# Optimization experiments

Measured on AMD Instinct MI355X. Metric: run time of the kernel, lower is better.

Reference implementation:

```python
import jax, jax.numpy as jnp
import numpy as np
from jax import lax

NEG = -1e30  # safe -inf surrogate (avoids nan grads)
CTC_WEIGHT = 0.3


def _excl_cumsum(e):
    # exclusive cumsum along last axis: (..., U) -> (..., U+1)
    c = jnp.cumsum(e, axis=-1)
    return jnp.concatenate([jnp.zeros_like(c[..., :1]), c], axis=-1)


def _rnnt_loss(log_probs, targets, frame_len, tgt_len, blank):
    """RNNT forward DP. log_probs: (B,T,U+1,V) log-softmaxed. Returns per-seq NLL (B,)."""
    B, T, U1, V = log_probs.shape
    blank_lp = log_probs[..., blank]  # (B,T,U1)
    emit = jnp.take_along_axis(log_probs[:, :, :U1 - 1, :],
                               targets[:, None, :, None], axis=3)[..., 0]  # (B,T,U)
    # alpha[0,u] = sum_{j<u} emit[0,j]
    alpha0 = _excl_cumsum(emit[:, 0])  # (B,U1)

    def step(alpha_prev, inp):
        blank_prev, emit_t = inp  # (B,U1), (B,U)
        a = alpha_prev + blank_prev
        # alpha[t,u] = LSE(a_u, alpha[t,u-1] + emit[t,u-1]) solved in closed form:
        # alpha[t,u] = E[u] + cumLSE_{k<=u}(a_k - E[k]),  E = exclusive cumsum of emit
        E = _excl_cumsum(emit_t)
        alpha_t = E + lax.associative_scan(jnp.logaddexp, a - E, axis=-1)
        return alpha_t, alpha_t

    xs = (jnp.swapaxes(blank_lp[:, :-1], 0, 1), jnp.swapaxes(emit[:, 1:], 0, 1))
    _, alphas = lax.scan(step, alpha0, xs)
    alphas = jnp.concatenate([alpha0[None], alphas], axis=0)  # (T,B,U1)
    bi = jnp.arange(B)
    t_idx = frame_len - 1
    ll = alphas[t_idx, bi, tgt_len] + blank_lp[bi, t_idx, tgt_len]
    return -ll


def _ctc_loss(log_probs, targets, frame_len, tgt_len, blank):
    """CTC forward DP. log_probs: (B,T,V) log-softmaxed. Returns per-seq NLL (B,)."""
    B, T, V = log_probs.shape
    U = targets.shape[1]
    S = 2 * U + 1
    ext = jnp.full((B, S), blank, dtype=targets.dtype).at[:, 1::2].set(targets)  # (B,S)
    lp_ext = jnp.take_along_axis(log_probs, ext[:, None, :], axis=2)  # (B,T,S)
    ext_m2 = jnp.pad(ext[:, :-2], ((0, 0), (2, 0)), constant_values=blank)
    can_skip = (jnp.arange(S)[None, :] >= 2) & (ext != blank) & (ext != ext_m2)
    alpha0 = jnp.full((B, S), NEG).at[:, 0].set(lp_ext[:, 0, 0]).at[:, 1].set(lp_ext[:, 0, 1])

    def step(alpha, lp_t):
        p1 = jnp.pad(alpha[:, :-1], ((0, 0), (1, 0)), constant_values=NEG)
        p2 = jnp.where(can_skip,
                       jnp.pad(alpha[:, :-2], ((0, 0), (2, 0)), constant_values=NEG), NEG)
        m = jnp.maximum(jnp.maximum(alpha, p1), p2)
        new = lp_t + m + jnp.log(jnp.exp(alpha - m) + jnp.exp(p1 - m) + jnp.exp(p2 - m))
        return new, new

    _, alphas = lax.scan(step, alpha0, jnp.swapaxes(lp_ext, 0, 1)[1:])
    alphas = jnp.concatenate([alpha0[None], alphas], axis=0)  # (T,B,S)
    bi = jnp.arange(B)
    t_idx = frame_len - 1
    a_last = alphas[t_idx, bi, 2 * tgt_len]
    a_prev = alphas[t_idx, bi, 2 * tgt_len - 1]
    return -jnp.logaddexp(a_last, a_prev)


def setup_inputs() -> dict:
    key = jax.random.key(0)
    ks = jax.random.split(key, 9)
    B, T, U, V = 4, 200, 50, 1024
    D, H = 512, 640
    return {
        "x_enc": jax.random.normal(ks[0], (B, T, D), jnp.float32),
        "x_dec": jax.random.normal(ks[1], (B, U + 1, H), jnp.float32),
        "target": jax.random.randint(ks[2], (B, U), 0, V - 1),  # excludes blank = V-1
        "frame_length": jax.random.randint(ks[3], (B,), 150, T + 1).astype(jnp.int32),
        "target_length": jax.random.randint(ks[4], (B,), 30, U + 1).astype(jnp.int32),
        "W_ctc": jax.random.normal(ks[5], (D, V), jnp.float32) * 0.02,
        "b_ctc": jnp.zeros((V,), jnp.float32),
        "W_enc": jax.random.normal(ks[6], (D, H), jnp.float32) * 0.02,
        "W_pred": jax.random.normal(ks[7], (H, H), jnp.float32) * 0.02,
        "b_joint": jnp.zeros((H,), jnp.float32),
        "W_out": jax.random.normal(ks[8], (H, V), jnp.float32) * 0.02,
        "b_out": jnp.zeros((V,), jnp.float32),
    }


def reference(x_enc, x_dec, target, frame_length, target_length,
              W_ctc, b_ctc, W_enc, W_pred, b_joint, W_out, b_out):
    B = x_enc.shape[0]
    V = W_ctc.shape[1]
    blank = V - 1
    # CTC head: linear + log_softmax over vocab
    ctc_lp = jax.nn.log_softmax(x_enc @ W_ctc + b_ctc, axis=-1)  # (B,T,V)
    # Joiner: enc proj (B,T,1,J) + pred proj (B,1,U+1,J) -> tanh -> vocab
    joint = jnp.tanh(jnp.einsum('btd,dj->btj', x_enc, W_enc)[:, :, None, :]
                     + jnp.einsum('buh,hj->buj', x_dec, W_pred)[:, None, :, :]
                     + b_joint)  # (B,T,U+1,J)
    rnnt_lp = jax.nn.log_softmax(jnp.einsum('btuj,jv->btuv', joint, W_out) + b_out, axis=-1)
    rnnt = _rnnt_loss(rnnt_lp, target, frame_length, target_length, blank).mean()
    ctc = _ctc_loss(ctc_lp, target, frame_length, target_length, blank).sum() / B
    return rnnt + CTC_WEIGHT * ctc
```

## Files before the change

kernel.cpp:

```cpp
#include <hip/hip_runtime.h>
#include <hip/hip_bf16.h>

typedef __bf16 bf16_t;
typedef __attribute__((ext_vector_type(8))) __bf16 bf16x8;
typedef __attribute__((ext_vector_type(4))) float f32x4;
typedef __attribute__((ext_vector_type(8))) int i32x8;
typedef __attribute__((ext_vector_type(4))) int i32x4;

#define NEGV (-1e30f)

#define BB 4
#define TT 200
#define UU 50
#define U1 51
#define VV 1024
#define DD 512
#define HH 640
#define RTOT (BB*TT*U1)
#define NBLK 638
#define SS 101

__device__ __forceinline__ float lae(float a, float b) {
    float mx = fmaxf(a, b);
    return mx + __logf(__expf(a - mx) + __expf(b - mx));
}
__device__ __forceinline__ float lae3(float a, float b, float c) {
    float mx = fmaxf(fmaxf(a, b), c);
    return mx + __logf(__expf(a - mx) + __expf(b - mx) + __expf(c - mx));
}
__device__ __forceinline__ float tanh_rcp(float x) {
    x = fminf(fmaxf(x, -10.f), 10.f);
    float ex = __expf(2.f * x);
    float r = __builtin_amdgcn_rcpf(ex + 1.f);
    return (ex - 1.f) * r;
}

__device__ __forceinline__ void pack_seg(const float* __restrict__ W, bf16_t* __restrict__ Wf,
                                         int e, int K32, int N)
{
    int j  = e & 7;
    int l  = (e >> 3) & 63;
    int kk = (e >> 9) % K32;
    int nt = e / (K32 * 512);
    int v = nt * 16 + (l & 15);
    int k = kk * 32 + ((l >> 4) << 2) + (j & 3) + ((j >> 2) << 4);
    Wf[e] = (bf16_t)W[(size_t)k * N + v];
}

__device__ __forceinline__ void pack_out8_mx(const float* __restrict__ W, unsigned* __restrict__ Wf8,
                                             int e32)
{
    int w4   = e32 & 7;
    int l    = (e32 >> 3) & 63;
    int ksnt = e32 >> 9;
    int ks   = ksnt % 5;
    int nt   = ksnt / 5;
    int v = nt * 16 + (l & 15);
    int kb = ks * 128 + ((l >> 4) << 5) + w4 * 4;
    float f[4];
#pragma unroll
    for (int t = 0; t < 4; ++t) f[t] = W[(size_t)(kb + t) * VV + v] * 16.f;
    unsigned r = __builtin_amdgcn_cvt_pk_fp8_f32(f[0], f[1], 0, false);
    r = __builtin_amdgcn_cvt_pk_fp8_f32(f[2], f[3], r, true);
    Wf8[e32] = r;
}

__global__ void pack_bf16(const float* __restrict__ Wenc, const float* __restrict__ Wpred,
                          const float* __restrict__ Wctc,
                          bf16_t* __restrict__ FEnc, bf16_t* __restrict__ FPred,
                          bf16_t* __restrict__ FCtc, float* __restrict__ out)
{
    if (blockIdx.x == 0 && threadIdx.x == 0) out[0] = 0.f;
    int e = blockIdx.x * 256 + threadIdx.x;
    if (e < 327680) { pack_seg(Wenc, FEnc, e, 16, 640); return; }
    e -= 327680;
    if (e < 409600) { pack_seg(Wpred, FPred, e, 20, 640); return; }
    e -= 409600;
    pack_seg(Wctc, FCtc, e, 16, 1024);
}

template<int K32, int L, bool LSE, int J>
__device__ void gemm_dev(const float* __restrict__ A, int M, int rowbase, int K,
                         const bf16_t* __restrict__ Wf, const float* __restrict__ bias,
                         float* __restrict__ C, float* __restrict__ lse_out, int N,
                         bf16_t* Atile, float (*ps)[8])
{
    const int tid = threadIdx.x;
#pragma unroll
    for (int it = 0; it < J * K32 / 8; ++it) {
        int fi = it * 512 + tid;
        int l = fi & 63, jk = fi >> 6;
        int j = jk / K32, kk = jk - j * K32;
        int row = rowbase + j * 16 + (l & 15);
        if (row > M - 1) row = M - 1;
        int c0 = kk * 32 + ((l >> 4) << 2);
        const float4 a0 = *(const float4*)&A[(size_t)row * K + c0];
        const float4 a1 = *(const float4*)&A[(size_t)row * K + c0 + 16];
        bf16x8 v;
        v[0] = (bf16_t)a0.x; v[1] = (bf16_t)a0.y; v[2] = (bf16_t)a0.z; v[3] = (bf16_t)a0.w;
        v[4] = (bf16_t)a1.x; v[5] = (bf16_t)a1.y; v[6] = (bf16_t)a1.z; v[7] = (bf16_t)a1.w;
        *(bf16x8*)&Atile[(size_t)fi * 8] = v;
    }
    __syncthreads();

    const int l = tid & 63, w = tid >> 6;
    const int lrow = l & 15, lhi = l >> 4;

    f32x4 acc[J][L];
#pragma unroll
    for (int j = 0; j < J; ++j)
#pragma unroll
        for (int li = 0; li < L; ++li) acc[j][li] = f32x4{0.f, 0.f, 0.f, 0.f};

    for (int kk = 0; kk < K32; ++kk) {
        bf16x8 a[J];
#pragma unroll
        for (int j = 0; j < J; ++j)
            a[j] = *(const bf16x8*)&Atile[(size_t)(((j * K32 + kk) * 64 + l) * 8)];
#pragma unroll
        for (int li = 0; li < L; ++li) {
            bf16x8 b = *(const bf16x8*)&Wf[(size_t)(((w * L + li) * K32 + kk) * 64 + l) * 8];
#pragma unroll
            for (int j = 0; j < J; ++j)
                acc[j][li] = __builtin_amdgcn_mfma_f32_16x16x32_bf16(a[j], b, acc[j][li], 0, 0, 0);
        }
    }

    float se[J][4];
    if (LSE) {
#pragma unroll
        for (int j = 0; j < J; ++j)
#pragma unroll
            for (int i = 0; i < 4; ++i) se[j][i] = 0.f;
    }
#pragma unroll
    for (int j = 0; j < J; ++j)
#pragma unroll
        for (int li = 0; li < L; ++li) {
            int col = (w * L + li) * 16 + lrow;
            float bv = bias ? bias[col] : 0.f;
#pragma unroll
            for (int i = 0; i < 4; ++i) {
                int grow = rowbase + 16 * j + lhi * 4 + i;
                float x = acc[j][li][i] + bv;
                if (grow < M) C[(size_t)grow * N + col] = x;
                if (LSE) se[j][i] += __expf(x);
            }
        }
    if (LSE) {
#pragma unroll
        for (int d = 1; d < 16; d <<= 1)
#pragma unroll
            for (int j = 0; j < J; ++j)
#pragma unroll
                for (int i = 0; i < 4; ++i) se[j][i] += __shfl_xor(se[j][i], d);
        if (lrow == 0) {
#pragma unroll
            for (int j = 0; j < J; ++j)
#pragma unroll
                for (int i = 0; i < 4; ++i) ps[16 * j + lhi * 4 + i][w] = se[j][i];
        }
        __syncthreads();
        if (tid < J * 16) {
            float s = 0.f;
#pragma unroll
            for (int w0 = 0; w0 < 8; ++w0) s += ps[tid][w0];
            int grow = rowbase + tid;
            if (grow < M) lse_out[grow] = __logf(s);
        }
    }
}

__global__ __launch_bounds__(512)
void mfma_gemm3(const float* __restrict__ x_enc, const float* __restrict__ x_dec,
                const bf16_t* __restrict__ FEnc, const bf16_t* __restrict__ FPred,
                const bf16_t* __restrict__ FCtc, const float* __restrict__ b_ctc,
                float* __restrict__ enc_proj, float* __restrict__ pred_proj,
                float* __restrict__ ctc_logits, float* __restrict__ ctc_lse,
                const float* __restrict__ Wout, unsigned* __restrict__ FOut8)
{
    __shared__ bf16_t Atile[2560 * 8];
    __shared__ float ps[64][8];
    int blk = blockIdx.x;
    if (blk >= 107) {
        int e = (blk - 107) * 512 + threadIdx.x;
        pack_out8_mx(Wout, FOut8, e);
        return;
    }
    if (blk < 50)
        gemm_dev<16, 5, false, 1>(x_enc, 800, blk * 16, 512, FEnc, nullptr, enc_proj, nullptr, 640, Atile, ps);
    else if (blk < 57)
        gemm_dev<20, 5, false, 2>(x_dec, 204, (blk - 50) * 32, 640, FPred, nullptr, pred_proj, nullptr, 640, Atile, ps);
    else
        gemm_dev<16, 8, true, 1>(x_enc, 800, (blk - 57) * 16, 512, FCtc, b_ctc, ctc_logits, ctc_lse, 1024, Atile, ps);
}

__global__ __launch_bounds__(512)
void joint_gemm(const float* __restrict__ enc,
                const float* __restrict__ pred,
                const float* __restrict__ bj,
                const unsigned* __restrict__ Wf8,
                const float* __restrict__ bo,
                const int* __restrict__ target,
                float* __restrict__ blank_buf, float* __restrict__ emit_buf)
{
    __shared__ __align__(16) char tile[64 * 656];
    __shared__ __align__(16) char Afrag8[40960];
    __shared__ const float* ep[64];
    __shared__ const float* pp[64];
    const int tid = threadIdx.x;
    const int blk = blockIdx.x;

    const int l = tid & 63, w = tid >> 6;
    const int lrow = l & 15, lhi = l >> 4;

    if (tid < 64) {
        int r = blk * 64 + tid; if (r > RTOT - 1) r = RTOT - 1;
        int b = r / (TT * U1); int rem = r - b * (TT * U1);
        int t = rem / U1;      int u = rem - t * U1;
        ep[tid] = enc + (size_t)(b * TT + t) * HH;
        pp[tid] = pred + (size_t)(b * U1 + u) * HH;
    }
    __syncthreads();

#pragma unroll 4
    for (int it = 0; it < 20; ++it) {
        int i = it * 512 + tid;
        int row = i / 160;
        int c4 = i - row * 160;
        int c0 = c4 * 4;
        const float4 e4 = *(const float4*)&ep[row][c0];
        const float4 p4 = *(const float4*)&pp[row][c0];
        const float4 q4 = *(const float4*)&bj[c0];
        float f0 = tanh_rcp(e4.x + p4.x + q4.x);
        float f1 = tanh_rcp(e4.y + p4.y + q4.y);
        float f2 = tanh_rcp(e4.z + p4.z + q4.z);
        float f3 = tanh_rcp(e4.w + p4.w + q4.w);
        unsigned r0 = __builtin_amdgcn_cvt_pk_fp8_f32(f0, f1, 0, false);
        unsigned v = __builtin_amdgcn_cvt_pk_fp8_f32(f2, f3, r0, true);
        *(unsigned*)&tile[row * 656 + c0] = v;
    }
    __syncthreads();

#pragma unroll
    for (int it = 0; it < 5; ++it) {
        int c = it * 512 + tid;
        int lA = c & 63;
        int plane = c >> 6;
        int h = plane & 1;
        int jks = plane >> 1;
        int ks = jks % 5;
        int j = jks / 5;
        int row = j * 16 + (lA & 15);
        int kbase = ks * 128 + ((lA >> 4) << 5) + h * 16;
        uint4 v = *(const uint4*)&tile[row * 656 + kbase];
        *(uint4*)&Afrag8[(size_t)c * 16] = v;
    }
    __syncthreads();

    f32x4 acc[4][8];
#pragma unroll
    for (int j = 0; j < 4; ++j)
#pragma unroll
        for (int li = 0; li < 8; ++li) acc[j][li] = f32x4{0.f, 0.f, 0.f, 0.f};

    const char* Bp8 = (const char*)Wf8 + (size_t)(w * 8) * 10240 + (size_t)l * 32;

    const int rot = blk % 5;
    auto kstep = [&](int ks) {
        i32x8 a[4];
#pragma unroll
        for (int j = 0; j < 4; ++j) {
            i32x4 lo = *(const i32x4*)(Afrag8 + (size_t)(((j * 5 + ks) * 2 + 0) * 1024 + l * 16));
            i32x4 hi = *(const i32x4*)(Afrag8 + (size_t)(((j * 5 + ks) * 2 + 1) * 1024 + l * 16));
            a[j][0] = lo[0]; a[j][1] = lo[1]; a[j][2] = lo[2]; a[j][3] = lo[3];
            a[j][4] = hi[0]; a[j][5] = hi[1]; a[j][6] = hi[2]; a[j][7] = hi[3];
        }
#pragma unroll
        for (int li = 0; li < 8; ++li) {
            i32x8 b = *(const i32x8*)(Bp8 + (size_t)li * 10240 + (size_t)ks * 2048);
#pragma unroll
            for (int j = 0; j < 4; ++j)
                acc[j][li] = __builtin_amdgcn_mfma_scale_f32_16x16x128_f8f6f4(
                    a[j], b, acc[j][li], 0, 0,
                    0, 0x7F7F7F7F, 0, 0x7F7F7F7F);
        }
    };
    for (int ks0 = rot; ks0 < 5; ++ks0) kstep(ks0);
    for (int ks0 = 0; ks0 < rot; ++ks0) kstep(ks0);

    int tg[4][4];
#pragma unroll
    for (int j = 0; j < 4; ++j)
#pragma unroll
        for (int i = 0; i < 4; ++i) {
            int r = blk * 64 + 16 * j + lhi * 4 + i; if (r > RTOT - 1) r = RTOT - 1;
            int b = r / (TT * U1); int rem = r - b * (TT * U1);
            int u = rem % U1;
            tg[j][i] = (u < UU) ? target[b * UU + u] : -1;
        }

    float se[4][4], ee[4][4], bbv[4][4];
#pragma unroll
    for (int j = 0; j < 4; ++j)
#pragma unroll
        for (int i = 0; i < 4; ++i) { se[j][i] = 0.f; ee[j][i] = NEGV; bbv[j][i] = NEGV; }

#pragma unroll
    for (int li = 0; li < 8; ++li) {
        int col = (w * 8 + li) * 16 + lrow;
        float bv = bo[col];
#pragma unroll
        for (int j = 0; j < 4; ++j)
#pragma unroll
            for (int i = 0; i < 4; ++i) {
                float x = acc[j][li][i] * 0.0625f + bv;
                se[j][i] += __expf(x);
                if (col == tg[j][i]) ee[j][i] = x;
            }
    }
    if (w == 7) {
        float bv = bo[1023];
#pragma unroll
        for (int j = 0; j < 4; ++j)
#pragma unroll
            for (int i = 0; i < 4; ++i) {
                float x = acc[j][7][i] * 0.0625f + bv;
                if (lrow == 15) bbv[j][i] = x;
            }
    }
#pragma unroll
    for (int d = 1; d < 16; d <<= 1)
#pragma unroll
        for (int j = 0; j < 4; ++j)
#pragma unroll
            for (int i = 0; i < 4; ++i) {
                se[j][i] += __shfl_xor(se[j][i], d);
                ee[j][i] = fmaxf(ee[j][i], __shfl_xor(ee[j][i], d));
                bbv[j][i] = fmaxf(bbv[j][i], __shfl_xor(bbv[j][i], d));
            }

    __syncthreads();
    float (*ps)[8] = (float (*)[8])(Afrag8);
    float (*pe)[8] = (float (*)[8])(Afrag8 + 2048);
    float (*pb)[8] = (float (*)[8])(Afrag8 + 4096);
    if (lrow == 0) {
#pragma unroll
        for (int j = 0; j < 4; ++j)
#pragma unroll
            for (int i = 0; i < 4; ++i) {
                int r = 16 * j + lhi * 4 + i;
                ps[r][w] = se[j][i]; pe[r][w] = ee[j][i]; pb[r][w] = bbv[j][i];
            }
    }
    __syncthreads();
    if (tid < 64) {
        float s = 0.f, e = NEGV, bq = NEGV;
#pragma unroll
        for (int w0 = 0; w0 < 8; ++w0) {
            s += ps[tid][w0];
            e = fmaxf(e, pe[tid][w0]);
            bq = fmaxf(bq, pb[tid][w0]);
        }
        float lse = __logf(s);
        int gid = blk * 64 + tid;
        if (gid < RTOT) {
            blank_buf[gid] = bq - lse;
            emit_buf[gid]  = e - lse;
        }
    }
}

__global__ __launch_bounds__(256)
void dp_fused(const float* __restrict__ blank_buf, const float* __restrict__ emit_buf,
              const float* __restrict__ ctc_logits, const float* __restrict__ ctc_lse,
              const int* __restrict__ target, const int* __restrict__ frame_len,
              const int* __restrict__ tgt_len,
              float* __restrict__ out)
{
    __shared__ __align__(16) float sm[28416];
    const int bid = blockIdx.x;
    const int tid = threadIdx.x;

    if (bid < 4) {
        const int b = bid;
        float2* pk = (float2*)sm;
        for (int i = tid; i < TT * U1; i += 256) {
            int t = i / U1, uu = i - t * U1;
            float bl = blank_buf[(b * TT + t) * U1 + uu];
            float em = emit_buf[(b * TT + t) * U1 + uu];
            pk[uu * 217 + t + 8] = make_float2(bl, em);
        }
        __syncthreads();
        if (tid >= 64) return;
        const int u = tid;
        const int fl = frame_len[b], tl = tgt_len[b];
        const int dh = fl - 1 + tl;
        const bool isTL = (u == tl);
        const bool act = (u < U1);
        float A = (u == 0) ? 0.f : NEGV;
        float Asave = (dh == 0 && isTL) ? A : NEGV;
        const float2* prow = pk + u * 217;

        for (int d0 = 1; d0 <= 249; d0 += 8) {
            int tb = d0 - 1 - u;
            int tc = tb; if (tc < -8) tc = -8; if (tc > 200) tc = 200;
            float2 buf[8];
#pragma unroll
            for (int s = 0; s < 8; ++s) buf[s] = prow[tc + 8 + s];
#pragma unroll
            for (int s = 0; s < 8; ++s) {
                int d = d0 + s;
                int t_new = d - u;
                float2 be = buf[s];
                float vshare = A + be.y;
                float left = __shfl_up(vshare, 1);
                if (u == 0) left = NEGV;
                float up = (t_new >= 1) ? (A + be.x) : NEGV;
                float Anew = lae(up, left);
                bool valid = act && (t_new >= 0) && (t_new < TT);
                A = valid ? Anew : A;
                Asave = (isTL && d == dh) ? A : Asave;
            }
        }
        if (isTL && act) {
            float bl = prow[(fl - 1) + 8].x;
            atomicAdd(out, -0.25f * (Asave + bl));
        }
    } else {
        const int b = bid - 4;
        float* lpE = sm;
        float* lpO = sm + 208;
        for (int i = tid; i < TT; i += 256) {
            int bt = b * TT + i;
            lpE[i] = ctc_logits[(size_t)bt * VV + (VV - 1)] - ctc_lse[bt];
        }
        for (int i = tid; i < TT * UU; i += 256) {
            int t = i / UU, uu = i - t * UU;
            int bt = b * TT + t;
            lpO[uu * 209 + t] = ctc_logits[(size_t)bt * VV + target[b * UU + uu]] - ctc_lse[bt];
        }
        __syncthreads();
        if (tid >= 64) return;
        const int u = tid;
        const int fl = frame_len[b], tl = tgt_len[b];
        const bool acte = (u <= 50);
        const bool acto = (u < 50);
        bool skip = (u >= 1 && u < UU) ? (target[b * UU + u] != target[b * UU + u - 1]) : false;
        const float* orow = lpO + u * 209;
        float old_e = (u == 0) ? lpE[0] : NEGV;
        float old_o = (u == 0) ? orow[0] : NEGV;
        float Esave = (fl == 1) ? old_e : NEGV;
        float Osave = (fl == 1) ? old_o : NEGV;

        for (int t0 = 1; t0 <= 193; t0 += 8) {
            float bo8[8], be8[8];
#pragma unroll
            for (int s = 0; s < 8; ++s) { bo8[s] = orow[t0 + s]; be8[s] = lpE[t0 + s]; }
#pragma unroll
            for (int s = 0; s < 8; ++s) {
                int t = t0 + s;
                float prev_o = __shfl_up(old_o, 1);
                if (u == 0) prev_o = NEGV;
                float ne = be8[s] + lae(old_e, prev_o);
                float no = bo8[s] + lae3(old_o, old_e, skip ? prev_o : NEGV);
                old_e = acte ? ne : NEGV;
                old_o = acto ? no : NEGV;
                bool hv = (t == fl - 1) && (t < TT);
                Esave = hv ? old_e : Esave;
                Osave = hv ? old_o : Osave;
            }
        }
        float a_last = __shfl(Esave, tl);
        float a_prev = __shfl(Osave, tl - 1);
        if (u == 0) atomicAdd(out, -0.075f * lae(a_last, a_prev));
    }
}

extern "C" void kernel_launch(void* const* d_in, const int* in_sizes, int n_in,
                              void* d_out, int out_size, void* d_ws, size_t ws_size,
                              hipStream_t stream)
{
    const float* x_enc   = (const float*)d_in[0];
    const float* x_dec   = (const float*)d_in[1];
    const int*   target  = (const int*)d_in[2];
    const int*   frame_l = (const int*)d_in[3];
    const int*   tgt_l   = (const int*)d_in[4];
    const float* W_ctc   = (const float*)d_in[5];
    const float* b_ctc   = (const float*)d_in[6];
    const float* W_enc   = (const float*)d_in[7];
    const float* W_pred  = (const float*)d_in[8];
    const float* b_joint = (const float*)d_in[9];
    const float* W_out   = (const float*)d_in[10];
    const float* b_out   = (const float*)d_in[11];
    float* out = (float*)d_out;

    float* wsf        = (float*)d_ws;
    float* enc_proj   = wsf;
    float* pred_proj  = wsf + 512000;
    float* ctc_logits = wsf + 642560;
    float* ctc_lse    = wsf + 1461760;
    float* blank_buf  = wsf + 1462592;
    float* emit_buf   = wsf + 1503424;
    unsigned* FOut8 = (unsigned*)(wsf + 1544272);
    bf16_t* FEnc  = (bf16_t*)(wsf + 1708112);
    bf16_t* FPred = (bf16_t*)(wsf + 1871952);
    bf16_t* FCtc  = (bf16_t*)(wsf + 2076752);

    pack_bf16<<<4928, 256, 0, stream>>>(W_enc, W_pred, W_ctc, FEnc, FPred, FCtc, out);
    mfma_gemm3<<<427, 512, 0, stream>>>(x_enc, x_dec, FEnc, FPred, FCtc, b_ctc,
                                        enc_proj, pred_proj, ctc_logits, ctc_lse,
                                        W_out, FOut8);
    joint_gemm<<<NBLK, 512, 0, stream>>>(enc_proj, pred_proj, b_joint, FOut8, b_out,
                                         target, blank_buf, emit_buf);
    dp_fused<<<8, 256, 0, stream>>>(blank_buf, emit_buf, ctc_logits, ctc_lse,
                                    target, frame_l, tgt_l, out);
}
```

Measured before the change: 150.2 us.

## Overlap CTC DP with joint GEMM and vectorize bf16 weight packing

Moves the CTC forward DP out of the final DP kernel and into four extra blocks appended to the joint GEMM launch. The CTC recursion, which only needs the CTC logits, can then run concurrently with the joiner instead of serially after it. The bf16 weight pack kernel now has each thread produce 8 packed elements written with one vector store, cutting the grid eightfold. Risks: the joint kernel grows its shared allocation to a single union buffer, and the extra long-running serial blocks could extend the joint kernel's tail.

```diff
diff --git a/kernel.cpp b/kernel.cpp
--- a/kernel.cpp
+++ b/kernel.cpp
@@ -35,18 +35,6 @@
     return (ex - 1.f) * r;
 }
 
-__device__ __forceinline__ void pack_seg(const float* __restrict__ W, bf16_t* __restrict__ Wf,
-                                         int e, int K32, int N)
-{
-    int j  = e & 7;
-    int l  = (e >> 3) & 63;
-    int kk = (e >> 9) % K32;
-    int nt = e / (K32 * 512);
-    int v = nt * 16 + (l & 15);
-    int k = kk * 32 + ((l >> 4) << 2) + (j & 3) + ((j >> 2) << 4);
-    Wf[e] = (bf16_t)W[(size_t)k * N + v];
-}
-
 __device__ __forceinline__ void pack_out8_mx(const float* __restrict__ W, unsigned* __restrict__ Wf8,
                                              int e32)
 {
@@ -71,12 +59,23 @@
                           bf16_t* __restrict__ FCtc, float* __restrict__ out)
 {
     if (blockIdx.x == 0 && threadIdx.x == 0) out[0] = 0.f;
-    int e = blockIdx.x * 256 + threadIdx.x;
-    if (e < 327680) { pack_seg(Wenc, FEnc, e, 16, 640); return; }
-    e -= 327680;
-    if (e < 409600) { pack_seg(Wpred, FPred, e, 20, 640); return; }
-    e -= 409600;
-    pack_seg(Wctc, FCtc, e, 16, 1024);
+    int f = blockIdx.x * 256 + threadIdx.x;
+    const float* W; bf16_t* Wf; int K32, N;
+    if (f < 40960)      { W = Wenc;  Wf = FEnc;  K32 = 16; N = 640; }
+    else if (f < 92160) { f -= 40960; W = Wpred; Wf = FPred; K32 = 20; N = 640; }
+    else                { f -= 92160; W = Wctc;  Wf = FCtc;  K32 = 16; N = 1024; }
+    int l  = f & 63;
+    int kk = (f >> 6) % K32;
+    int nt = f / (64 * K32);
+    int v  = nt * 16 + (l & 15);
+    int kb = kk * 32 + ((l >> 4) << 2);
+    bf16x8 o;
+#pragma unroll
+    for (int j = 0; j < 8; ++j) {
+        int k = kb + (j & 3) + ((j >> 2) << 4);
+        o[j] = (bf16_t)W[(size_t)k * N + v];
+    }
+    *(bf16x8*)&Wf[(size_t)f * 8] = o;
 }
 
 template<int K32, int L, bool LSE, int J>
@@ -202,15 +201,69 @@
                 const unsigned* __restrict__ Wf8,
                 const float* __restrict__ bo,
                 const int* __restrict__ target,
-                float* __restrict__ blank_buf, float* __restrict__ emit_buf)
-{
-    __shared__ __align__(16) char tile[64 * 656];
-    __shared__ __align__(16) char Afrag8[40960];
+                float* __restrict__ blank_buf, float* __restrict__ emit_buf,
+                const float* __restrict__ ctc_logits, const float* __restrict__ ctc_lse,
+                const int* __restrict__ frame_len, const int* __restrict__ tgt_len,
+                float* __restrict__ out)
+{
+    __shared__ __align__(16) char smem[84992];
     __shared__ const float* ep[64];
     __shared__ const float* pp[64];
     const int tid = threadIdx.x;
     const int blk = blockIdx.x;
 
+    if (blk >= NBLK) {
+        const int b = blk - NBLK;
+        float* lpE = (float*)smem;
+        float* lpO = (float*)smem + 208;
+        for (int i = tid; i < TT; i += 512) {
+            int bt = b * TT + i;
+            lpE[i] = ctc_logits[(size_t)bt * VV + (VV - 1)] - ctc_lse[bt];
+        }
+        for (int i = tid; i < TT * UU; i += 512) {
+            int t = i / UU, uu = i - t * UU;
+            int bt = b * TT + t;
+            lpO[uu * 209 + t] = ctc_logits[(size_t)bt * VV + target[b * UU + uu]] - ctc_lse[bt];
+        }
+        __syncthreads();
+        if (tid >= 64) return;
+        const int u = tid;
+        const int fl = frame_len[b], tl = tgt_len[b];
+        const bool acte = (u <= 50);
+        const bool acto = (u < 50);
+        bool skip = (u >= 1 && u < UU) ? (target[b * UU + u] != target[b * UU + u - 1]) : false;
+        const float* orow = lpO + u * 209;
+        float old_e = (u == 0) ? lpE[0] : NEGV;
+        float old_o = (u == 0) ? orow[0] : NEGV;
+        float Esave = (fl == 1) ? old_e : NEGV;
+        float Osave = (fl == 1) ? old_o : NEGV;
+
+        for (int t0 = 1; t0 <= 193; t0 += 8) {
+            float bo8[8], be8[8];
+#pragma unroll
+            for (int s = 0; s < 8; ++s) { bo8[s] = orow[t0 + s]; be8[s] = lpE[t0 + s]; }
+#pragma unroll
+            for (int s = 0; s < 8; ++s) {
+                int t = t0 + s;
+                float prev_o = __shfl_up(old_o, 1);
+                if (u == 0) prev_o = NEGV;
+                float ne = be8[s] + lae(old_e, prev_o);
+                float no = bo8[s] + lae3(old_o, old_e, skip ? prev_o : NEGV);
+                old_e = acte ? ne : NEGV;
+                old_o = acto ? no : NEGV;
+                bool hv = (t == fl - 1) && (t < TT);
+                Esave = hv ? old_e : Esave;
+                Osave = hv ? old_o : Osave;
+            }
+        }
+        float a_last = __shfl(Esave, tl);
+        float a_prev = __shfl(Osave, tl - 1);
+        if (u == 0) atomicAdd(out, -0.075f * lae(a_last, a_prev));
+        return;
+    }
+
+    char* tile = smem;
+    char* Afrag8 = smem + 41984;
     const int l = tid & 63, w = tid >> 6;
     const int lrow = l & 15, lhi = l >> 4;
 
@@ -372,108 +425,56 @@
 }
 
 __global__ __launch_bounds__(256)
-void dp_fused(const float* __restrict__ blank_buf, const float* __restrict__ emit_buf,
-              const float* __restrict__ ctc_logits, const float* __restrict__ ctc_lse,
-              const int* __restrict__ target, const int* __restrict__ frame_len,
-              const int* __restrict__ tgt_len,
-              float* __restrict__ out)
+void dp_rnnt(const float* __restrict__ blank_buf, const float* __restrict__ emit_buf,
+             const int* __restrict__ frame_len, const int* __restrict__ tgt_len,
+             float* __restrict__ out)
 {
     __shared__ __align__(16) float sm[28416];
-    const int bid = blockIdx.x;
+    const int b = blockIdx.x;
     const int tid = threadIdx.x;
 
-    if (bid < 4) {
-        const int b = bid;
-        float2* pk = (float2*)sm;
-        for (int i = tid; i < TT * U1; i += 256) {
-            int t = i / U1, uu = i - t * U1;
-            float bl = blank_buf[(b * TT + t) * U1 + uu];
-            float em = emit_buf[(b * TT + t) * U1 + uu];
-            pk[uu * 217 + t + 8] = make_float2(bl, em);
-        }
-        __syncthreads();
-        if (tid >= 64) return;
-        const int u = tid;
-        const int fl = frame_len[b], tl = tgt_len[b];
-        const int dh = fl - 1 + tl;
-        const bool isTL = (u == tl);
-        const bool act = (u < U1);
-        float A = (u == 0) ? 0.f : NEGV;
-        float Asave = (dh == 0 && isTL) ? A : NEGV;
-        const float2* prow = pk + u * 217;
-
-        for (int d0 = 1; d0 <= 249; d0 += 8) {
-            int tb = d0 - 1 - u;
-            int tc = tb; if (tc < -8) tc = -8; if (tc > 200) tc = 200;
-            float2 buf[8];
-#pragma unroll
-            for (int s = 0; s < 8; ++s) buf[s] = prow[tc + 8 + s];
-#pragma unroll
-            for (int s = 0; s < 8; ++s) {
-                int d = d0 + s;
-                int t_new = d - u;
-                float2 be = buf[s];
-                float vshare = A + be.y;
-                float left = __shfl_up(vshare, 1);
-                if (u == 0) left = NEGV;
-                float up = (t_new >= 1) ? (A + be.x) : NEGV;
-                float Anew = lae(up, left);
-                bool valid = act && (t_new >= 0) && (t_new < TT);
-                A = valid ? Anew : A;
-                Asave = (isTL && d == dh) ? A : Asave;
-            }
-        }
-        if (isTL && act) {
-            float bl = prow[(fl - 1) + 8].x;
-            atomicAdd(out, -0.25f * (Asave + bl));
-        }
-    } else {
-        const int b = bid - 4;
-        float* lpE = sm;
-        float* lpO = sm + 208;
-        for (int i = tid; i < TT; i += 256) {
-            int bt = b * TT + i;
-            lpE[i] = ctc_logits[(size_t)bt * VV + (VV - 1)] - ctc_lse[bt];
-        }
-        for (int i = tid; i < TT * UU; i += 256) {
-            int t = i / UU, uu = i - t * UU;
-            int bt = b * TT + t;
-            lpO[uu * 209 + t] = ctc_logits[(size_t)bt * VV + target[b * UU + uu]] - ctc_lse[bt];
-        }
-        __syncthreads();
-        if (tid >= 64) return;
-        const int u = tid;
-        const int fl = frame_len[b], tl = tgt_len[b];
-        const bool acte = (u <= 50);
-        const bool acto = (u < 50);
-        bool skip = (u >= 1 && u < UU) ? (target[b * UU + u] != target[b * UU + u - 1]) : false;
-        const float* orow = lpO + u * 209;
-        float old_e = (u == 0) ? lpE[0] : NEGV;
-        float old_o = (u == 0) ? orow[0] : NEGV;
-        float Esave = (fl == 1) ? old_e : NEGV;
-        float Osave = (fl == 1) ? old_o : NEGV;
-
-        for (int t0 = 1; t0 <= 193; t0 += 8) {
-            float bo8[8], be8[8];
-#pragma unroll
-            for (int s = 0; s < 8; ++s) { bo8[s] = orow[t0 + s]; be8[s] = lpE[t0 + s]; }
-#pragma unroll
-            for (int s = 0; s < 8; ++s) {
-                int t = t0 + s;
-                float prev_o = __shfl_up(old_o, 1);
-                if (u == 0) prev_o = NEGV;
-                float ne = be8[s] + lae(old_e, prev_o);
-                float no = bo8[s] + lae3(old_o, old_e, skip ? prev_o : NEGV);
-                old_e = acte ? ne : NEGV;
-                old_o = acto ? no : NEGV;
-                bool hv = (t == fl - 1) && (t < TT);
-                Esave = hv ? old_e : Esave;
-                Osave = hv ? old_o : Osave;
-            }
-        }
-        float a_last = __shfl(Esave, tl);
-        float a_prev = __shfl(Osave, tl - 1);
-        if (u == 0) atomicAdd(out, -0.075f * lae(a_last, a_prev));
+    float2* pk = (float2*)sm;
+    for (int i = tid; i < TT * U1; i += 256) {
+        int t = i / U1, uu = i - t * U1;
+        float bl = blank_buf[(b * TT + t) * U1 + uu];
+        float em = emit_buf[(b * TT + t) * U1 + uu];
+        pk[uu * 217 + t + 8] = make_float2(bl, em);
+    }
+    __syncthreads();
+    if (tid >= 64) return;
+    const int u = tid;
+    const int fl = frame_len[b], tl = tgt_len[b];
+    const int dh = fl - 1 + tl;
+    const bool isTL = (u == tl);
+    const bool act = (u < U1);
+    float A = (u == 0) ? 0.f : NEGV;
+    float Asave = (dh == 0 && isTL) ? A : NEGV;
+    const float2* prow = pk + u * 217;
+
+    for (int d0 = 1; d0 <= 249; d0 += 8) {
+        int tb = d0 - 1 - u;
+        int tc = tb; if (tc < -8) tc = -8; if (tc > 200) tc = 200;
+        float2 buf[8];
+#pragma unroll
+        for (int s = 0; s < 8; ++s) buf[s] = prow[tc + 8 + s];
+#pragma unroll
+        for (int s = 0; s < 8; ++s) {
+            int d = d0 + s;
+            int t_new = d - u;
+            float2 be = buf[s];
+            float vshare = A + be.y;
+            float left = __shfl_up(vshare, 1);
+            if (u == 0) left = NEGV;
+            float up = (t_new >= 1) ? (A + be.x) : NEGV;
+            float Anew = lae(up, left);
+            bool valid = act && (t_new >= 0) && (t_new < TT);
+            A = valid ? Anew : A;
+            Asave = (isTL && d == dh) ? A : Asave;
+        }
+    }
+    if (isTL && act) {
+        float bl = prow[(fl - 1) + 8].x;
+        atomicAdd(out, -0.25f * (Asave + bl));
     }
 }
 
@@ -507,12 +508,12 @@
     bf16_t* FPred = (bf16_t*)(wsf + 1871952);
     bf16_t* FCtc  = (bf16_t*)(wsf + 2076752);
 
-    pack_bf16<<<4928, 256, 0, stream>>>(W_enc, W_pred, W_ctc, FEnc, FPred, FCtc, out);
+    pack_bf16<<<616, 256, 0, stream>>>(W_enc, W_pred, W_ctc, FEnc, FPred, FCtc, out);
     mfma_gemm3<<<427, 512, 0, stream>>>(x_enc, x_dec, FEnc, FPred, FCtc, b_ctc,
                                         enc_proj, pred_proj, ctc_logits, ctc_lse,
                                         W_out, FOut8);
-    joint_gemm<<<NBLK, 512, 0, stream>>>(enc_proj, pred_proj, b_joint, FOut8, b_out,
-                                         target, blank_buf, emit_buf);
-    dp_fused<<<8, 256, 0, stream>>>(blank_buf, emit_buf, ctc_logits, ctc_lse,
-                                    target, frame_l, tgt_l, out);
-}
+    joint_gemm<<<NBLK + 4, 512, 0, stream>>>(enc_proj, pred_proj, b_joint, FOut8, b_out,
+                                             target, blank_buf, emit_buf,
+                                             ctc_logits, ctc_lse, frame_l, tgt_l, out);
+    dp_rnnt<<<4, 256, 0, stream>>>(blank_buf, emit_buf, frame_l, tgt_l, out);
+}
```

Result: slower. 164.8 us (+9.7%).
